# Kernel optimization log

Measured on AMD Instinct MI355X. Metric: run time of the kernel, lower is better.

## Reference

```python
import jax, jax.numpy as jnp
import numpy as np

D = 1024
N_HEAD = 16
D_HEAD = D // N_HEAD
B, S = 4, 2048
EPS = 1e-6


def rmsnorm(x, w):
    # x: [..., d_head]
    return x / jnp.sqrt(jnp.mean(x * x, axis=-1, keepdims=True) + EPS) * w


def setup_inputs() -> dict:
    key = jax.random.key(0)
    ks = jax.random.split(key, 6)
    x = jax.random.normal(ks[0], (B, S, D), dtype=jnp.float32)
    # causal mask: True means masked (upper triangle above diagonal)
    mask = jnp.triu(jnp.ones((S, S), dtype=bool), k=1)
    scale = 1.0 / np.sqrt(D)
    W_qkv = jax.random.normal(ks[1], (D, 3 * D), dtype=jnp.float32) * scale
    b_qkv = jnp.zeros((3 * D,), dtype=jnp.float32)
    W_o = jax.random.normal(ks[2], (D, D), dtype=jnp.float32) * scale
    b_o = jnp.zeros((D,), dtype=jnp.float32)
    wq = jnp.ones((D_HEAD,), dtype=jnp.float32)
    wk = jnp.ones((D_HEAD,), dtype=jnp.float32)
    return {"x": x, "mask": mask, "W_qkv": W_qkv, "b_qkv": b_qkv,
            "W_o": W_o, "b_o": b_o, "wq": wq, "wk": wk}


def reference(x, mask, W_qkv, b_qkv, W_o, b_o, wq, wk):
    b, s, d = x.shape
    qkv = x @ W_qkv + b_qkv  # [b,s,3d]
    q, k, v = jnp.split(qkv, 3, axis=-1)
    q = q.reshape(b, s, N_HEAD, D_HEAD)
    k = k.reshape(b, s, N_HEAD, D_HEAD)
    v = v.reshape(b, s, N_HEAD, D_HEAD)
    q = rmsnorm(q, wq)
    k = rmsnorm(k, wk)
    # NOTE: no 1/sqrt(d_head) scaling, faithful to the source
    attn = jnp.einsum('bqhd,bkhd->bhqk', q, k)
    attn = jnp.where(mask[None, None, :, :], -jnp.inf, attn)
    attn = jax.nn.softmax(attn, axis=-1)
    z = jnp.einsum('bhqk,bkhd->bqhd', attn, v).reshape(b, s, d)
    return z @ W_o + b_o
```

## Files before the change

kernel.cpp:

```cpp
#include <hip/hip_runtime.h>
#include <cmath>

typedef _Float16 half_t;
typedef _Float16 half8 __attribute__((ext_vector_type(8)));
typedef _Float16 half4v __attribute__((ext_vector_type(4)));
typedef float float4v __attribute__((ext_vector_type(4)));

#define LOG2E 1.44269504088896340736f

#define GLDS16(g, l)                                                                   \
    __builtin_amdgcn_global_load_lds((const __attribute__((address_space(1))) void*)(g), \
                                     (__attribute__((address_space(3))) void*)(l), 16, 0, 0)

#define BAR_LGKM() __asm__ volatile("s_waitcnt lgkmcnt(0)\n\ts_barrier" ::: "memory")
#define BAR_VM(n)  __asm__ volatile("s_waitcnt vmcnt(" #n ")\n\ts_barrier" ::: "memory")

__global__ void cast_f32_f16(const float* __restrict__ in, half_t* __restrict__ out, int n) {
    int i = (blockIdx.x * blockDim.x + threadIdx.x) * 4;
    if (i >= n) return;
    float4 v = *(const float4*)(in + i);
    half4v o;
    o[0] = (half_t)v.x; o[1] = (half_t)v.y; o[2] = (half_t)v.z; o[3] = (half_t)v.w;
    *(half4v*)(out + i) = o;
}

__global__ void transpose_cast(const float* __restrict__ in, half_t* __restrict__ out, int R, int C) {
    __shared__ float tile[32][33];
    int c0 = blockIdx.x * 32, r0 = blockIdx.y * 32;
    int tx = threadIdx.x, ty = threadIdx.y;
    for (int p = 0; p < 4; p++) {
        int r = r0 + ty + p * 8;
        tile[ty + p * 8][tx] = in[(size_t)r * C + c0 + tx];
    }
    __syncthreads();
    for (int p = 0; p < 4; p++) {
        int c = c0 + ty + p * 8;
        out[(size_t)c * R + r0 + tx] = (half_t)tile[tx][ty + p * 8];
    }
}

template <int MODE>
__global__ __launch_bounds__(256, 3) void gemm_f16(
    const half_t* __restrict__ A,
    const half_t* __restrict__ Bt,
    const float* __restrict__ bias,
    void* __restrict__ Cout,
    int M, int N, int K,
    const float* __restrict__ wq, const float* __restrict__ wk,
    half_t* __restrict__ Qh, half_t* __restrict__ Kh)
{
    __shared__ __align__(16) half_t As[3][128 * 32];
    __shared__ __align__(16) half_t Bs[3][128 * 32];
    int t = threadIdx.x;
    int lane = t & 63, w = t >> 6;
    int m0 = blockIdx.x * 128, n0 = blockIdx.y * 128;
    int wm = (w >> 1) * 64, wn = (w & 1) * 64;
    int lrow = lane & 15, quad = lane >> 4;

    int lc = ((t & 3) - (t >> 3)) & 3;
    const half_t* gA = A  + (size_t)(m0 + (t >> 2)) * K + lc * 8;
    const half_t* gB = Bt + (size_t)(n0 + (t >> 2)) * K + lc * 8;
    half_t* ldsA[3] = { &As[0][w * 512], &As[1][w * 512], &As[2][w * 512] };
    half_t* ldsB[3] = { &Bs[0][w * 512], &Bs[1][w * 512], &Bs[2][w * 512] };

    int posq = (quad + (lrow >> 1)) & 3;

    float4v acc[4][4] = {};

    GLDS16(gA,                       ldsA[0]);
    GLDS16(gA + (size_t)64 * K,      ldsA[0] + 2048);
    GLDS16(gB,                       ldsB[0]);
    GLDS16(gB + (size_t)64 * K,      ldsB[0] + 2048);
    GLDS16(gA + 32,                  ldsA[1]);
    GLDS16(gA + (size_t)64 * K + 32, ldsA[1] + 2048);
    GLDS16(gB + 32,                  ldsB[1]);
    GLDS16(gB + (size_t)64 * K + 32, ldsB[1] + 2048);

    int nk = K >> 5;
    for (int ki = 0; ki < nk; ki++) {
        int cur = ki % 3, pre = (ki + 2) % 3;
        BAR_LGKM();
        if (ki + 2 < nk) {
            int kp = (ki + 2) << 5;
            GLDS16(gA + kp,                  ldsA[pre]);
            GLDS16(gA + (size_t)64 * K + kp, ldsA[pre] + 2048);
            GLDS16(gB + kp,                  ldsB[pre]);
            GLDS16(gB + (size_t)64 * K + kp, ldsB[pre] + 2048);
            BAR_VM(8);
        } else if (ki + 1 < nk) {
            BAR_VM(4);
        } else {
            BAR_VM(0);
        }
        half8 af[4], bf[4];
        for (int i = 0; i < 4; i++) af[i] = *(const half8*)(&As[cur][(wm + i * 16 + lrow) * 32 + posq * 8]);
        for (int i = 0; i < 4; i++) bf[i] = *(const half8*)(&Bs[cur][(wn + i * 16 + lrow) * 32 + posq * 8]);
        for (int mi = 0; mi < 4; mi++)
            for (int ni = 0; ni < 4; ni++)
                acc[mi][ni] = __builtin_amdgcn_mfma_f32_16x16x32_f16(af[mi], bf[ni], acc[mi][ni], 0, 0, 0);
    }

    if (MODE == 0) {
        float* out = (float*)Cout;
        for (int mi = 0; mi < 4; mi++)
            for (int ni = 0; ni < 4; ni++)
                for (int r = 0; r < 4; r++) {
                    int gr = m0 + wm + mi * 16 + quad * 4 + r;
                    int gc = n0 + wn + ni * 16 + lrow;
                    out[(size_t)gr * N + gc] = acc[mi][ni][r] + bias[gc];
                }
    } else {
        int nglob = n0 + wn;
        if (nglob < 2048) {
            int isK = nglob >> 10;
            int h = (nglob >> 6) & 15;
            const float* wv = isK ? wk : wq;
            half_t* dst = isK ? Kh : Qh;
            float post = isK ? 1.0f : LOG2E;
            for (int mi = 0; mi < 4; mi++)
                for (int r = 0; r < 4; r++) {
                    int gr = m0 + wm + mi * 16 + quad * 4 + r;
                    float v[4]; float ss = 0.f;
                    for (int ni = 0; ni < 4; ni++) {
                        v[ni] = acc[mi][ni][r] + bias[nglob + ni * 16 + lrow];
                        ss += v[ni] * v[ni];
                    }
                    ss += __shfl_xor(ss, 1);
                    ss += __shfl_xor(ss, 2);
                    ss += __shfl_xor(ss, 4);
                    ss += __shfl_xor(ss, 8);
                    float rr = rsqrtf(ss * (1.0f / 64.0f) + 1e-6f) * post;
                    int bb = gr >> 11, s = gr & 2047;
                    size_t rowbase = ((size_t)((bb * 16 + h) * 2048 + s)) * 64;
                    for (int ni = 0; ni < 4; ni++) {
                        int d = ni * 16 + lrow;
                        dst[rowbase + d] = (half_t)(v[ni] * rr * wv[d]);
                    }
                }
        } else {
            half_t* Vt = (half_t*)Cout;
            for (int mi = 0; mi < 4; mi++) {
                int gr = m0 + wm + mi * 16 + quad * 4;
                int bb = gr >> 11, s = gr & 2047;
                for (int ni = 0; ni < 4; ni++) {
                    int dg = nglob + ni * 16 + lrow - 2048;
                    float bv = bias[nglob + ni * 16 + lrow];
                    half4v oh;
                    for (int r = 0; r < 4; r++) oh[r] = (half_t)(acc[mi][ni][r] + bv);
                    *(half4v*)(Vt + ((size_t)((bb * 16 + (dg >> 6)) * 64 + (dg & 63))) * 2048 + s) = oh;
                }
            }
        }
    }
}

__global__ __launch_bounds__(512, 4) void attn(
    const half_t* __restrict__ Qh, const half_t* __restrict__ Kh, const half_t* __restrict__ Vt,
    half_t* __restrict__ Z)
{
    __shared__ __align__(16) half_t Ks[2][64 * 64];
    __shared__ __align__(16) half_t Vs[2][64 * 64];
    __shared__ __align__(16) half_t Ps[8 * 16 * 64];

    int bh = blockIdx.x;
    int b = bh >> 4, h = bh & 15;
    int t = threadIdx.x, lane = t & 63, w = t >> 6;
    int lrow = lane & 15, quad = lane >> 4;

    int sr = w * 8 + (lane >> 3);
    int scc = (lane & 7) ^ ((lane >> 3) & 7);
    const half_t* gK0 = Kh + ((size_t)bh * 2048 + sr) * 64 + scc * 8;
    const half_t* gV0 = Vt + ((size_t)bh * 64 + sr) * 2048 + scc * 8;

    int sw = lrow & 7;
    int cA = (quad ^ sw) * 8;
    int cB = ((quad + 4) ^ sw) * 8;
    half_t* PsW = Ps + w * 1024 + lrow * 64;

    for (int pass = 0; pass < 2; pass++) {
        int qt = pass ? (15 - (int)blockIdx.y) : (int)blockIdx.y;
        int q0w = qt * 128 + w * 16;

        const half_t* Qbase = Qh + ((size_t)bh * 2048 + q0w + lrow) * 64;
        half8 qf0 = *(const half8*)(Qbase + quad * 8);
        half8 qf1 = *(const half8*)(Qbase + 32 + quad * 8);

        float4v ot[4] = {};
        float m = -__builtin_inff(), l = 0.f;

        int nt = 2 * qt + 2;
        __syncthreads();
        GLDS16(gK0, &Ks[0][w * 512]);
        GLDS16(gV0, &Vs[0][w * 512]);

        for (int kt = 0; kt < nt; kt++) {
            int cur = kt & 1, nxt = cur ^ 1;
            int kb = kt * 64;
            BAR_LGKM();
            if (kt + 1 < nt) {
                GLDS16(gK0 + (size_t)(kb + 64) * 64, &Ks[nxt][w * 512]);
                GLDS16(gV0 + kb + 64,                &Vs[nxt][w * 512]);
                BAR_VM(2);
            } else {
                BAR_VM(0);
            }
            if (kb > q0w + 15) continue;

            float4v st[4];
            for (int f = 0; f < 4; f++) {
                float4v z = {};
                const half_t* kr = &Ks[cur][(f * 16 + lrow) * 64];
                half8 k0 = *(const half8*)(kr + cA);
                half8 k1 = *(const half8*)(kr + cB);
                z = __builtin_amdgcn_mfma_f32_16x16x32_f16(k0, qf0, z, 0, 0, 0);
                z = __builtin_amdgcn_mfma_f32_16x16x32_f16(k1, qf1, z, 0, 0, 0);
                st[f] = z;
            }
            if (kb + 63 > q0w) {
                int qabs = q0w + lrow;
                for (int f = 0; f < 4; f++)
                    for (int r = 0; r < 4; r++) {
                        int key = kb + f * 16 + quad * 4 + r;
                        if (key > qabs) st[f][r] = -__builtin_inff();
                    }
            }
            float tm = st[0][0];
            for (int f = 0; f < 4; f++)
                for (int r = 0; r < 4; r++) tm = fmaxf(tm, st[f][r]);
            tm = fmaxf(tm, __shfl_xor(tm, 16));
            tm = fmaxf(tm, __shfl_xor(tm, 32));
            float mn = fmaxf(m, tm);
            float alpha = __builtin_amdgcn_exp2f(m - mn);
            m = mn;
            float rs = 0.f;
            for (int f = 0; f < 4; f++) {
                float p0 = __builtin_amdgcn_exp2f(st[f][0] - mn);
                float p1 = __builtin_amdgcn_exp2f(st[f][1] - mn);
                float p2 = __builtin_amdgcn_exp2f(st[f][2] - mn);
                float p3 = __builtin_amdgcn_exp2f(st[f][3] - mn);
                rs += (p0 + p1) + (p2 + p3);
                uint2 pw;
                pw.x = __builtin_bit_cast(unsigned, __builtin_amdgcn_cvt_pkrtz(p0, p1));
                pw.y = __builtin_bit_cast(unsigned, __builtin_amdgcn_cvt_pkrtz(p2, p3));
                int cc = (2 * f + (quad >> 1)) ^ sw;
                *(uint2*)(PsW + cc * 8 + (quad & 1) * 4) = pw;
            }
            rs += __shfl_xor(rs, 16);
            rs += __shfl_xor(rs, 32);
            l = l * alpha + rs;
            for (int f2 = 0; f2 < 4; f2++)
                for (int r = 0; r < 4; r++) ot[f2][r] *= alpha;

            __asm__ volatile("s_waitcnt lgkmcnt(0)" ::: "memory");
            half8 p0v = *(const half8*)(PsW + cA);
            half8 p1v = *(const half8*)(PsW + cB);
            for (int f2 = 0; f2 < 4; f2++) {
                const half_t* vr = &Vs[cur][(f2 * 16 + lrow) * 64];
                half8 v0 = *(const half8*)(vr + cA);
                half8 v1 = *(const half8*)(vr + cB);
                ot[f2] = __builtin_amdgcn_mfma_f32_16x16x32_f16(v0, p0v, ot[f2], 0, 0, 0);
                ot[f2] = __builtin_amdgcn_mfma_f32_16x16x32_f16(v1, p1v, ot[f2], 0, 0, 0);
            }
        }

        float inv = 1.0f / l;
        size_t base = ((size_t)(b * 2048) + q0w + lrow) * 1024 + h * 64;
        for (int f2 = 0; f2 < 4; f2++) {
            half4v oh;
            for (int r = 0; r < 4; r++) oh[r] = (half_t)(ot[f2][r] * inv);
            *(half4v*)(Z + base + f2 * 16 + quad * 4) = oh;
        }
    }
}

extern "C" void kernel_launch(void* const* d_in, const int* in_sizes, int n_in,
                              void* d_out, int out_size, void* d_ws, size_t ws_size,
                              hipStream_t stream)
{
    const float* x     = (const float*)d_in[0];
    const float* W_qkv = (const float*)d_in[2];
    const float* b_qkv = (const float*)d_in[3];
    const float* W_o   = (const float*)d_in[4];
    const float* b_o   = (const float*)d_in[5];
    const float* wq    = (const float*)d_in[6];
    const float* wk    = (const float*)d_in[7];
    float* out = (float*)d_out;

    char* ws = (char*)d_ws;
    half_t* xh   = (half_t*)(ws);
    half_t* Wqt  = (half_t*)(ws + (16ull << 20));
    half_t* Wot  = (half_t*)(ws + (22ull << 20));
    half_t* Qh   = (half_t*)(ws + (40ull << 20));
    half_t* Kh   = (half_t*)(ws + (56ull << 20));
    half_t* Vt   = (half_t*)(ws + (72ull << 20));
    half_t* zh   = xh;

    cast_f32_f16<<<8192, 256, 0, stream>>>(x, xh, 8192 * 1024);
    transpose_cast<<<dim3(96, 32), dim3(32, 8), 0, stream>>>(W_qkv, Wqt, 1024, 3072);
    transpose_cast<<<dim3(32, 32), dim3(32, 8), 0, stream>>>(W_o, Wot, 1024, 1024);
    gemm_f16<1><<<dim3(64, 24), 256, 0, stream>>>(xh, Wqt, b_qkv, Vt, 8192, 3072, 1024,
                                                  wq, wk, Qh, Kh);
    attn<<<dim3(64, 8), 512, 0, stream>>>(Qh, Kh, Vt, zh);
    gemm_f16<0><<<dim3(64, 8), 256, 0, stream>>>(zh, Wot, b_o, out, 8192, 1024, 1024,
                                                 nullptr, nullptr, nullptr, nullptr);
}
```

Measured before the change: 272.6 us.

## Double attention key/value tile to 128 keys per iteration

The causal attention kernel now processes 128 keys per loop iteration instead of 64. This halves the number of double-buffered K/V load stages and the barriers between them. The softmax probabilities are staged through the per-warp LDS buffer in two 64-key halves so the existing P·V MFMA structure can be reused. In exchange, LDS use per block doubles, which may lower occupancy. The early skip for fully masked tiles is gone, so warps do extra masked work on the diagonal tile.

```diff
diff --git a/kernel.cpp b/kernel.cpp
--- a/kernel.cpp
+++ b/kernel.cpp
@@ -158,24 +158,29 @@
     const half_t* __restrict__ Qh, const half_t* __restrict__ Kh, const half_t* __restrict__ Vt,
     half_t* __restrict__ Z)
 {
-    __shared__ __align__(16) half_t Ks[2][64 * 64];
-    __shared__ __align__(16) half_t Vs[2][64 * 64];
-    __shared__ __align__(16) half_t Ps[8 * 16 * 64];
+    __shared__ __align__(16) half_t Ks[2][128 * 64];
+    __shared__ __align__(16) half_t Vs[2][64 * 128];
+    __shared__ __align__(16) half_t Ps[8][16 * 64];
 
     int bh = blockIdx.x;
     int b = bh >> 4, h = bh & 15;
     int t = threadIdx.x, lane = t & 63, w = t >> 6;
     int lrow = lane & 15, quad = lane >> 4;
 
-    int sr = w * 8 + (lane >> 3);
     int scc = (lane & 7) ^ ((lane >> 3) & 7);
-    const half_t* gK0 = Kh + ((size_t)bh * 2048 + sr) * 64 + scc * 8;
-    const half_t* gV0 = Vt + ((size_t)bh * 64 + sr) * 2048 + scc * 8;
+    const half_t* gK0 = Kh + ((size_t)bh * 2048 + w * 16 + (lane >> 3)) * 64 + scc * 8;
+    int vr0 = w * 8 + (lane >> 4);
+    int vc0 = (lane & 15) ^ (lane >> 4);
+    int vc1 = (lane & 15) ^ ((lane >> 4) + 4);
+    const half_t* gV0 = Vt + ((size_t)bh * 64 + vr0) * 2048 + vc0 * 8;
+    const half_t* gV1 = Vt + ((size_t)bh * 64 + vr0 + 4) * 2048 + vc1 * 8;
+    half_t* ldsK[2] = { &Ks[0][w * 1024], &Ks[1][w * 1024] };
+    half_t* ldsV[2] = { &Vs[0][w * 1024], &Vs[1][w * 1024] };
 
     int sw = lrow & 7;
     int cA = (quad ^ sw) * 8;
     int cB = ((quad + 4) ^ sw) * 8;
-    half_t* PsW = Ps + w * 1024 + lrow * 64;
+    half_t* PsW = &Ps[w][lrow * 64];
 
     for (int pass = 0; pass < 2; pass++) {
         int qt = pass ? (15 - (int)blockIdx.y) : (int)blockIdx.y;
@@ -188,26 +193,30 @@
         float4v ot[4] = {};
         float m = -__builtin_inff(), l = 0.f;
 
-        int nt = 2 * qt + 2;
+        int nt = qt + 1;
         __syncthreads();
-        GLDS16(gK0, &Ks[0][w * 512]);
-        GLDS16(gV0, &Vs[0][w * 512]);
+        GLDS16(gK0,       ldsK[0]);
+        GLDS16(gK0 + 512, ldsK[0] + 512);
+        GLDS16(gV0,       ldsV[0]);
+        GLDS16(gV1,       ldsV[0] + 512);
 
         for (int kt = 0; kt < nt; kt++) {
             int cur = kt & 1, nxt = cur ^ 1;
-            int kb = kt * 64;
+            int kb = kt * 128;
             BAR_LGKM();
             if (kt + 1 < nt) {
-                GLDS16(gK0 + (size_t)(kb + 64) * 64, &Ks[nxt][w * 512]);
-                GLDS16(gV0 + kb + 64,                &Vs[nxt][w * 512]);
-                BAR_VM(2);
+                size_t ko = (size_t)(kb + 128);
+                GLDS16(gK0 + ko * 64,       ldsK[nxt]);
+                GLDS16(gK0 + ko * 64 + 512, ldsK[nxt] + 512);
+                GLDS16(gV0 + ko,            ldsV[nxt]);
+                GLDS16(gV1 + ko,            ldsV[nxt] + 512);
+                BAR_VM(4);
             } else {
                 BAR_VM(0);
             }
-            if (kb > q0w + 15) continue;
-
-            float4v st[4];
-            for (int f = 0; f < 4; f++) {
+
+            float4v st[8];
+            for (int f = 0; f < 8; f++) {
                 float4v z = {};
                 const half_t* kr = &Ks[cur][(f * 16 + lrow) * 64];
                 half8 k0 = *(const half8*)(kr + cA);
@@ -216,16 +225,16 @@
                 z = __builtin_amdgcn_mfma_f32_16x16x32_f16(k1, qf1, z, 0, 0, 0);
                 st[f] = z;
             }
-            if (kb + 63 > q0w) {
+            if (kb + 127 > q0w) {
                 int qabs = q0w + lrow;
-                for (int f = 0; f < 4; f++)
+                for (int f = 0; f < 8; f++)
                     for (int r = 0; r < 4; r++) {
                         int key = kb + f * 16 + quad * 4 + r;
                         if (key > qabs) st[f][r] = -__builtin_inff();
                     }
             }
             float tm = st[0][0];
-            for (int f = 0; f < 4; f++)
+            for (int f = 0; f < 8; f++)
                 for (int r = 0; r < 4; r++) tm = fmaxf(tm, st[f][r]);
             tm = fmaxf(tm, __shfl_xor(tm, 16));
             tm = fmaxf(tm, __shfl_xor(tm, 32));
@@ -233,7 +242,8 @@
             float alpha = __builtin_amdgcn_exp2f(m - mn);
             m = mn;
             float rs = 0.f;
-            for (int f = 0; f < 4; f++) {
+            uint2 pw1[4];
+            for (int f = 0; f < 8; f++) {
                 float p0 = __builtin_amdgcn_exp2f(st[f][0] - mn);
                 float p1 = __builtin_amdgcn_exp2f(st[f][1] - mn);
                 float p2 = __builtin_amdgcn_exp2f(st[f][2] - mn);
@@ -242,8 +252,12 @@
                 uint2 pw;
                 pw.x = __builtin_bit_cast(unsigned, __builtin_amdgcn_cvt_pkrtz(p0, p1));
                 pw.y = __builtin_bit_cast(unsigned, __builtin_amdgcn_cvt_pkrtz(p2, p3));
-                int cc = (2 * f + (quad >> 1)) ^ sw;
-                *(uint2*)(PsW + cc * 8 + (quad & 1) * 4) = pw;
+                if (f < 4) {
+                    int cc = (2 * f + (quad >> 1)) ^ sw;
+                    *(uint2*)(PsW + cc * 8 + (quad & 1) * 4) = pw;
+                } else {
+                    pw1[f - 4] = pw;
+                }
             }
             rs += __shfl_xor(rs, 16);
             rs += __shfl_xor(rs, 32);
@@ -255,11 +269,25 @@
             half8 p0v = *(const half8*)(PsW + cA);
             half8 p1v = *(const half8*)(PsW + cB);
             for (int f2 = 0; f2 < 4; f2++) {
-                const half_t* vr = &Vs[cur][(f2 * 16 + lrow) * 64];
-                half8 v0 = *(const half8*)(vr + cA);
-                half8 v1 = *(const half8*)(vr + cB);
+                int row = f2 * 16 + lrow;
+                half8 v0 = *(const half8*)(&Vs[cur][row * 128 + ((quad ^ sw)) * 8]);
+                half8 v1 = *(const half8*)(&Vs[cur][row * 128 + (((4 + quad) ^ sw)) * 8]);
                 ot[f2] = __builtin_amdgcn_mfma_f32_16x16x32_f16(v0, p0v, ot[f2], 0, 0, 0);
                 ot[f2] = __builtin_amdgcn_mfma_f32_16x16x32_f16(v1, p1v, ot[f2], 0, 0, 0);
+            }
+            for (int f = 0; f < 4; f++) {
+                int cc = (2 * f + (quad >> 1)) ^ sw;
+                *(uint2*)(PsW + cc * 8 + (quad & 1) * 4) = pw1[f];
+            }
+            __asm__ volatile("s_waitcnt lgkmcnt(0)" ::: "memory");
+            half8 p2v = *(const half8*)(PsW + cA);
+            half8 p3v = *(const half8*)(PsW + cB);
+            for (int f2 = 0; f2 < 4; f2++) {
+                int row = f2 * 16 + lrow;
+                half8 v2 = *(const half8*)(&Vs[cur][row * 128 + (((8 + quad) ^ sw)) * 8]);
+                half8 v3 = *(const half8*)(&Vs[cur][row * 128 + (((12 + quad) ^ sw)) * 8]);
+                ot[f2] = __builtin_amdgcn_mfma_f32_16x16x32_f16(v2, p2v, ot[f2], 0, 0, 0);
+                ot[f2] = __builtin_amdgcn_mfma_f32_16x16x32_f16(v3, p3v, ot[f2], 0, 0, 0);
             }
         }
 
```

Result: no change. 272.5 us (-0.0%).
